# Optimization experiments

Hardware: AMD Instinct MI355X
Metric: run time of the kernel (lower is better)

The kernel has to match this reference:

```python
import jax, jax.numpy as jnp
import numpy as np

B = 524288
H = 64  # hidden_dim
D = 1   # input_dim


def setup_inputs() -> dict:
    key = jax.random.key(0)
    ks = jax.random.split(key, 16)
    s = 0.05
    inp = {
        "gradients": jax.random.normal(ks[0], (B, D), jnp.float32),
        "parameters": jax.random.normal(ks[1], (B, D), jnp.float32),
        "momentum": jax.random.normal(ks[2], (B, D), jnp.float32),
        "h0": jax.random.normal(ks[3], (B, H), jnp.float32),
        "c0": jax.random.normal(ks[4], (B, H), jnp.float32),
        # input_processor: Linear(3D->H), ReLU, Linear(H->H)
        "W1": jax.random.normal(ks[5], (H, 3 * D), jnp.float32) * s,
        "b1": jax.random.normal(ks[6], (H,), jnp.float32) * s,
        "W2": jax.random.normal(ks[7], (H, H), jnp.float32) * s,
        "b2": jax.random.normal(ks[8], (H,), jnp.float32) * s,
        # LSTM cell (PyTorch layout: gates stacked i,f,g,o -> 4H rows)
        "W_ih": jax.random.normal(ks[9], (4 * H, H), jnp.float32) * s,
        "W_hh": jax.random.normal(ks[10], (4 * H, H), jnp.float32) * s,
        "b_ih": jax.random.normal(ks[11], (4 * H,), jnp.float32) * s,
        "b_hh": jax.random.normal(ks[12], (4 * H,), jnp.float32) * s,
        # output_layer: Linear(H->D)
        "W_out": jax.random.normal(ks[13], (D, H), jnp.float32) * s,
        "b_out": jax.random.normal(ks[14], (D,), jnp.float32) * s,
    }
    return inp


def reference(gradients, parameters, momentum, h0, c0,
              W1, b1, W2, b2, W_ih, W_hh, b_ih, b_hh, W_out, b_out):
    # momentum update
    m = 0.9 * momentum + gradients                      # [B, D]
    feats = jnp.concatenate([gradients, parameters, m], axis=-1)  # [B, 3D]
    # small MLP
    x = jax.nn.relu(feats @ W1.T + b1) @ W2.T + b2      # [B, H]
    # single-step LSTM cell, PyTorch gate order i, f, g, o
    gates = x @ W_ih.T + b_ih + h0 @ W_hh.T + b_hh      # [B, 4H]
    i, f, g, o = jnp.split(gates, 4, axis=-1)
    c1 = jax.nn.sigmoid(f) * c0 + jax.nn.sigmoid(i) * jnp.tanh(g)
    h1 = jax.nn.sigmoid(o) * jnp.tanh(c1)               # [B, H]
    update = h1 @ W_out.T + b_out                       # [B, D]
    return update
```

## Files before the change

kernel.cpp:

```cpp
#include <hip/hip_runtime.h>
#include <hip/hip_bf16.h>
#include <stdint.h>


typedef __attribute__((ext_vector_type(8))) __bf16  bf16x8;
typedef __attribute__((ext_vector_type(4))) float   floatx4;

__device__ __forceinline__ unsigned short f2bf_bits(float x){
    unsigned u = __builtin_bit_cast(unsigned, x);
    u = u + 0x7fffu + ((u >> 16) & 1u);
    return (unsigned short)(u >> 16);
}
__device__ __forceinline__ unsigned pk2(float lo, float hi){
    return ((unsigned)f2bf_bits(hi) << 16) | (unsigned)f2bf_bits(lo);
}
__device__ __forceinline__ bf16x8 pack8(float4 a, float4 b){
    union { unsigned u[4]; bf16x8 v; } p;
    p.u[0] = pk2(a.x, a.y); p.u[1] = pk2(a.z, a.w);
    p.u[2] = pk2(b.x, b.y); p.u[3] = pk2(b.z, b.w);
    return p.v;
}
__device__ __forceinline__ float sigm(float x){
    float e = __builtin_amdgcn_exp2f(-1.442695041f * x);
    return __builtin_amdgcn_rcpf(1.0f + e);
}
__device__ __forceinline__ float tanh_fast(float x){
    float e = __builtin_amdgcn_exp2f(2.885390082f * x);
    return 1.0f - 2.0f * __builtin_amdgcn_rcpf(1.0f + e);
}

__global__ __launch_bounds__(256) void prep_kernel(
    const float* __restrict__ W2, const float* __restrict__ b2,
    const float* __restrict__ W_ih, const float* __restrict__ W_hh,
    const float* __restrict__ b_ih, const float* __restrict__ b_hh,
    unsigned short* __restrict__ wc, float* __restrict__ biasc)
{
    __shared__ float W2s[64*64];
    __shared__ float b2s[64];
    __shared__ float wihs[16*64];
    const int tid = threadIdx.x;
    const int b   = blockIdx.x;

    for (int i = 0; i < 4; i++){
        int idx = i*1024 + tid*4;
        *(float4*)(W2s + idx) = *(const float4*)(W2 + idx);
    }
    if (tid < 64) b2s[tid] = b2[tid];
    {
        int idx = tid*4;
        *(float4*)(wihs + idx) = *(const float4*)(W_ih + b*16*64 + idx);
    }
    __syncthreads();

    const int nl = tid >> 4;
    const int n  = b*16 + nl;
    const int jg = tid & 15;
    const int j  = jg*4;
    const int T  = n >> 4;

    float a0=0.f, a1=0.f, a2=0.f, a3=0.f;
    for (int h = 0; h < 64; h++){
        float wv = wihs[nl*64 + h];
        const float* w2r = W2s + h*64 + j;
        a0 += wv*w2r[0]; a1 += wv*w2r[1]; a2 += wv*w2r[2]; a3 += wv*w2r[3];
    }
    auto store4 = [&](int k, float v0, float v1, float v2, float v3){
        int s    = k >> 5;
        int lane = ((k >> 3) & 3)*16 + (n & 15);
        int off  = (T*4 + s)*512 + lane*8 + (k & 7);
        ushort4 v; v.x=f2bf_bits(v0); v.y=f2bf_bits(v1); v.z=f2bf_bits(v2); v.w=f2bf_bits(v3);
        *(ushort4*)(wc + off) = v;
    };
    store4(j, a0, a1, a2, a3);
    {
        const float* src = W_hh + n*64 + j;
        store4(64 + j, src[0], src[1], src[2], src[3]);
    }
    if (jg == 0){
        float s = b_ih[n] + b_hh[n];
        for (int h = 0; h < 64; h++) s += wihs[nl*64 + h]*b2s[h];
        biasc[n] = s;
    }
}

__global__ __launch_bounds__(512, 4) void main_kernel(
    const float* __restrict__ grad, const float* __restrict__ param,
    const float* __restrict__ mom,  const float* __restrict__ h0,
    const float* __restrict__ c0,   const float* __restrict__ W1,
    const float* __restrict__ b1,   const float* __restrict__ Wout,
    const float* __restrict__ bout,
    const unsigned short* __restrict__ wc, const float* __restrict__ biasc,
    float* __restrict__ out)
{
    __shared__ __align__(16) unsigned short wc_l[32768];
    __shared__ float  bias_l[256];
    __shared__ float4 w1p_l[64];

    const int tid  = threadIdx.x;
    const int lane = tid & 63;
    const int w    = tid >> 6;
    const int l15  = lane & 15;
    const int q    = lane >> 4;
    const long row0 = (long)blockIdx.x * 128;

    {
        const float4* src = (const float4*)wc;
        float4*       dst = (float4*)wc_l;
        #pragma unroll
        for (int i = 0; i < 8; i++)
            dst[i*512 + tid] = src[i*512 + tid];
    }
    if (tid < 256) bias_l[tid] = biasc[tid];
    if (tid >= 256 && tid < 320){
        int j = tid - 256;
        w1p_l[j] = make_float4(W1[j*3], W1[j*3+1], W1[j*3+2], b1[j]);
    }

    const long rA = row0 + w*16 + l15;
    float g = grad[rA], p = param[rA], mo = mom[rA];
    float m = 0.9f*mo + g;

    const float* hrow = h0 + rA*64;
    float4 ha = *(const float4*)(hrow + q*8);
    float4 hb = *(const float4*)(hrow + q*8 + 4);
    float4 hc = *(const float4*)(hrow + 32 + q*8);
    float4 hd = *(const float4*)(hrow + 32 + q*8 + 4);

    __syncthreads();

    float rv[16];
    #pragma unroll
    for (int s = 0; s < 2; s++)
        #pragma unroll
        for (int jj = 0; jj < 8; jj++){
            int j = s*32 + q*8 + jj;
            float4 wr = w1p_l[j];
            float v = fmaf(wr.x, g, fmaf(wr.y, p, fmaf(wr.z, m, wr.w)));
            rv[s*8+jj] = v > 0.f ? v : 0.f;
        }
    bf16x8 afr[4];
    afr[0] = pack8(make_float4(rv[0],rv[1],rv[2],rv[3]),
                   make_float4(rv[4],rv[5],rv[6],rv[7]));
    afr[1] = pack8(make_float4(rv[8],rv[9],rv[10],rv[11]),
                   make_float4(rv[12],rv[13],rv[14],rv[15]));
    afr[2] = pack8(ha, hb);
    afr[3] = pack8(hc, hd);

    floatx4 acc[16];
    #pragma unroll
    for (int T = 0; T < 16; T++){
        float bv = bias_l[T*16 + l15];
        const unsigned short* cb = wc_l + T*2048 + lane*8;
        bf16x8 b0 = *(const bf16x8*)(cb);
        bf16x8 b1f = *(const bf16x8*)(cb + 512);
        bf16x8 b2f = *(const bf16x8*)(cb + 1024);
        bf16x8 b3f = *(const bf16x8*)(cb + 1536);
        acc[T] = __builtin_amdgcn_mfma_f32_16x16x32_bf16(afr[0], b0,
                     (floatx4){bv, bv, bv, bv}, 0, 0, 0);
        acc[T] = __builtin_amdgcn_mfma_f32_16x16x32_bf16(afr[1], b1f, acc[T], 0, 0, 0);
        acc[T] = __builtin_amdgcn_mfma_f32_16x16x32_bf16(afr[2], b2f, acc[T], 0, 0, 0);
        acc[T] = __builtin_amdgcn_mfma_f32_16x16x32_bf16(afr[3], b3f, acc[T], 0, 0, 0);
    }

    const float* c0base = c0 + (row0 + w*16 + q*4)*64 + l15;
    float c0v[4][4];
    #pragma unroll
    for (int jh = 0; jh < 4; jh++)
        #pragma unroll
        for (int r = 0; r < 4; r++)
            c0v[jh][r] = c0base[r*64 + jh*16];

    float wo[4];
    #pragma unroll
    for (int jh = 0; jh < 4; jh++) wo[jh] = Wout[jh*16 + l15];
    const float bout0 = bout[0];

    float red[4] = {0.f, 0.f, 0.f, 0.f};
    #pragma unroll
    for (int jh = 0; jh < 4; jh++)
        #pragma unroll
        for (int r = 0; r < 4; r++){
            float iv = sigm(acc[jh][r]);
            float fv = sigm(acc[4+jh][r]);
            float gv = tanh_fast(acc[8+jh][r]);
            float ov = sigm(acc[12+jh][r]);
            float c1 = fmaf(fv, c0v[jh][r], iv*gv);
            float h1 = ov * tanh_fast(c1);
            red[r] = fmaf(h1, wo[jh], red[r]);
        }

    #pragma unroll
    for (int mset = 1; mset < 16; mset <<= 1)
        #pragma unroll
        for (int r = 0; r < 4; r++)
            red[r] += __shfl_xor(red[r], mset, 64);

    if (l15 == 0){
        long orow = row0 + w*16 + q*4;
        #pragma unroll
        for (int r = 0; r < 4; r++)
            out[orow + r] = red[r] + bout0;
    }
}

extern "C" void kernel_launch(void* const* d_in, const int* in_sizes, int n_in,
                              void* d_out, int out_size, void* d_ws, size_t ws_size,
                              hipStream_t stream)
{
    const float* grad  = (const float*)d_in[0];
    const float* param = (const float*)d_in[1];
    const float* mom   = (const float*)d_in[2];
    const float* h0    = (const float*)d_in[3];
    const float* c0    = (const float*)d_in[4];
    const float* W1    = (const float*)d_in[5];
    const float* b1    = (const float*)d_in[6];
    const float* W2    = (const float*)d_in[7];
    const float* b2    = (const float*)d_in[8];
    const float* W_ih  = (const float*)d_in[9];
    const float* W_hh  = (const float*)d_in[10];
    const float* b_ih  = (const float*)d_in[11];
    const float* b_hh  = (const float*)d_in[12];
    const float* Wout  = (const float*)d_in[13];
    const float* bout  = (const float*)d_in[14];

    unsigned short* wc = (unsigned short*)d_ws;
    float* biasc       = (float*)((char*)d_ws + 65536);

    prep_kernel<<<16, 256, 0, stream>>>(W2, b2, W_ih, W_hh, b_ih, b_hh, wc, biasc);

    const int nblocks = 524288 / 128;
    main_kernel<<<nblocks, 512, 0, stream>>>(grad, param, mom, h0, c0,
                                             W1, b1, Wout, bout, wc, biasc,
                                             (float*)d_out);
}
```

Baseline: 309.1 us.

## Make LSTM kernel persistent over row chunks with prefetch and per-hidden-slice gate MFMAs

The main kernel now uses 1024-thread blocks, each looping over four 256-row chunks. The next chunk's grad/param/mom/h0 loads are prefetched while the current chunk is computed. This amortizes the 64KB LDS weight staging over more rows and lets the gates be computed one hidden slice at a time (i,f,g,o per jh), so only four accumulators are live instead of sixteen, lowering register pressure. The bias is pre-scaled by the exp2 constant and folded into an fma, and bf16 packing uses a native vector convert. The risks are fewer blocks in the grid and a serialized jh loop that may expose MFMA and load latency.

```diff
diff --git a/kernel.cpp b/kernel.cpp
--- a/kernel.cpp
+++ b/kernel.cpp
@@ -4,6 +4,7 @@
 
 
 typedef __attribute__((ext_vector_type(8))) __bf16  bf16x8;
+typedef __attribute__((ext_vector_type(8))) float   f32x8;
 typedef __attribute__((ext_vector_type(4))) float   floatx4;
 
 __device__ __forceinline__ unsigned short f2bf_bits(float x){
@@ -11,22 +12,11 @@
     u = u + 0x7fffu + ((u >> 16) & 1u);
     return (unsigned short)(u >> 16);
 }
-__device__ __forceinline__ unsigned pk2(float lo, float hi){
-    return ((unsigned)f2bf_bits(hi) << 16) | (unsigned)f2bf_bits(lo);
-}
 __device__ __forceinline__ bf16x8 pack8(float4 a, float4 b){
-    union { unsigned u[4]; bf16x8 v; } p;
-    p.u[0] = pk2(a.x, a.y); p.u[1] = pk2(a.z, a.w);
-    p.u[2] = pk2(b.x, b.y); p.u[3] = pk2(b.z, b.w);
-    return p.v;
-}
-__device__ __forceinline__ float sigm(float x){
-    float e = __builtin_amdgcn_exp2f(-1.442695041f * x);
-    return __builtin_amdgcn_rcpf(1.0f + e);
-}
-__device__ __forceinline__ float tanh_fast(float x){
-    float e = __builtin_amdgcn_exp2f(2.885390082f * x);
-    return 1.0f - 2.0f * __builtin_amdgcn_rcpf(1.0f + e);
+    f32x8 t;
+    t[0]=a.x; t[1]=a.y; t[2]=a.z; t[3]=a.w;
+    t[4]=b.x; t[5]=b.y; t[6]=b.z; t[7]=b.w;
+    return __builtin_convertvector(t, bf16x8);
 }
 
 __global__ __launch_bounds__(256) void prep_kernel(
@@ -83,7 +73,7 @@
     }
 }
 
-__global__ __launch_bounds__(512, 4) void main_kernel(
+__global__ __launch_bounds__(1024, 4) void main_kernel(
     const float* __restrict__ grad, const float* __restrict__ param,
     const float* __restrict__ mom,  const float* __restrict__ h0,
     const float* __restrict__ c0,   const float* __restrict__ W1,
@@ -95,111 +85,157 @@
     __shared__ __align__(16) unsigned short wc_l[32768];
     __shared__ float  bias_l[256];
     __shared__ float4 w1p_l[64];
+    __shared__ float  wout_l[64];
 
     const int tid  = threadIdx.x;
     const int lane = tid & 63;
     const int w    = tid >> 6;
     const int l15  = lane & 15;
     const int q    = lane >> 4;
-    const long row0 = (long)blockIdx.x * 128;
 
     {
         const float4* src = (const float4*)wc;
         float4*       dst = (float4*)wc_l;
         #pragma unroll
-        for (int i = 0; i < 8; i++)
-            dst[i*512 + tid] = src[i*512 + tid];
-    }
-    if (tid < 256) bias_l[tid] = biasc[tid];
-    if (tid >= 256 && tid < 320){
+        for (int i = 0; i < 4; i++)
+            dst[i*1024 + tid] = src[i*1024 + tid];
+    }
+    if (tid < 256){
+        float sc = ((tid >> 6) == 2) ? 2.885390082f : -1.442695041f;
+        bias_l[tid] = sc * biasc[tid];
+    } else if (tid < 320){
         int j = tid - 256;
         w1p_l[j] = make_float4(W1[j*3], W1[j*3+1], W1[j*3+2], b1[j]);
-    }
-
-    const long rA = row0 + w*16 + l15;
-    float g = grad[rA], p = param[rA], mo = mom[rA];
-    float m = 0.9f*mo + g;
-
-    const float* hrow = h0 + rA*64;
-    float4 ha = *(const float4*)(hrow + q*8);
-    float4 hb = *(const float4*)(hrow + q*8 + 4);
-    float4 hc = *(const float4*)(hrow + 32 + q*8);
-    float4 hd = *(const float4*)(hrow + 32 + q*8 + 4);
+    } else if (tid < 384){
+        wout_l[tid - 320] = Wout[tid - 320];
+    }
+
+    const float bout0 = bout[0];
+    constexpr int NCH = 4;
+    const long blockBase = (long)blockIdx.x * (NCH * 256);
+
+    {
+        long rA = blockBase + w*16 + l15;
+    }
+    long rA0 = blockBase + w*16 + l15;
+    float g_r  = grad[rA0];
+    float p_r  = param[rA0];
+    float mo_r = mom[rA0];
+    const float* hr0 = h0 + rA0*64;
+    float4 ha = *(const float4*)(hr0 + q*8);
+    float4 hb = *(const float4*)(hr0 + q*8 + 4);
+    float4 hc = *(const float4*)(hr0 + 32 + q*8);
+    float4 hd = *(const float4*)(hr0 + 32 + q*8 + 4);
 
     __syncthreads();
 
-    float rv[16];
-    #pragma unroll
-    for (int s = 0; s < 2; s++)
+    const floatx4 zq = {0.f, 0.f, 0.f, 0.f};
+
+    #pragma unroll 1
+    for (int t = 0; t < NCH; ++t){
+        const long rowt = blockBase + t*256;
+
+        float m = fmaf(0.9f, mo_r, g_r);
+        f32x8 rlo, rhi;
         #pragma unroll
         for (int jj = 0; jj < 8; jj++){
-            int j = s*32 + q*8 + jj;
-            float4 wr = w1p_l[j];
-            float v = fmaf(wr.x, g, fmaf(wr.y, p, fmaf(wr.z, m, wr.w)));
-            rv[s*8+jj] = v > 0.f ? v : 0.f;
-        }
-    bf16x8 afr[4];
-    afr[0] = pack8(make_float4(rv[0],rv[1],rv[2],rv[3]),
-                   make_float4(rv[4],rv[5],rv[6],rv[7]));
-    afr[1] = pack8(make_float4(rv[8],rv[9],rv[10],rv[11]),
-                   make_float4(rv[12],rv[13],rv[14],rv[15]));
-    afr[2] = pack8(ha, hb);
-    afr[3] = pack8(hc, hd);
-
-    floatx4 acc[16];
-    #pragma unroll
-    for (int T = 0; T < 16; T++){
-        float bv = bias_l[T*16 + l15];
-        const unsigned short* cb = wc_l + T*2048 + lane*8;
-        bf16x8 b0 = *(const bf16x8*)(cb);
-        bf16x8 b1f = *(const bf16x8*)(cb + 512);
-        bf16x8 b2f = *(const bf16x8*)(cb + 1024);
-        bf16x8 b3f = *(const bf16x8*)(cb + 1536);
-        acc[T] = __builtin_amdgcn_mfma_f32_16x16x32_bf16(afr[0], b0,
-                     (floatx4){bv, bv, bv, bv}, 0, 0, 0);
-        acc[T] = __builtin_amdgcn_mfma_f32_16x16x32_bf16(afr[1], b1f, acc[T], 0, 0, 0);
-        acc[T] = __builtin_amdgcn_mfma_f32_16x16x32_bf16(afr[2], b2f, acc[T], 0, 0, 0);
-        acc[T] = __builtin_amdgcn_mfma_f32_16x16x32_bf16(afr[3], b3f, acc[T], 0, 0, 0);
-    }
-
-    const float* c0base = c0 + (row0 + w*16 + q*4)*64 + l15;
-    float c0v[4][4];
-    #pragma unroll
-    for (int jh = 0; jh < 4; jh++)
-        #pragma unroll
-        for (int r = 0; r < 4; r++)
-            c0v[jh][r] = c0base[r*64 + jh*16];
-
-    float wo[4];
-    #pragma unroll
-    for (int jh = 0; jh < 4; jh++) wo[jh] = Wout[jh*16 + l15];
-    const float bout0 = bout[0];
-
-    float red[4] = {0.f, 0.f, 0.f, 0.f};
-    #pragma unroll
-    for (int jh = 0; jh < 4; jh++)
-        #pragma unroll
-        for (int r = 0; r < 4; r++){
-            float iv = sigm(acc[jh][r]);
-            float fv = sigm(acc[4+jh][r]);
-            float gv = tanh_fast(acc[8+jh][r]);
-            float ov = sigm(acc[12+jh][r]);
-            float c1 = fmaf(fv, c0v[jh][r], iv*gv);
-            float h1 = ov * tanh_fast(c1);
-            red[r] = fmaf(h1, wo[jh], red[r]);
-        }
-
-    #pragma unroll
-    for (int mset = 1; mset < 16; mset <<= 1)
-        #pragma unroll
-        for (int r = 0; r < 4; r++)
-            red[r] += __shfl_xor(red[r], mset, 64);
-
-    if (l15 == 0){
-        long orow = row0 + w*16 + q*4;
-        #pragma unroll
-        for (int r = 0; r < 4; r++)
-            out[orow + r] = red[r] + bout0;
+            float4 wr = w1p_l[q*8 + jj];
+            float v = fmaf(wr.x, g_r, fmaf(wr.y, p_r, fmaf(wr.z, m, wr.w)));
+            rlo[jj] = v > 0.f ? v : 0.f;
+        }
+        #pragma unroll
+        for (int jj = 0; jj < 8; jj++){
+            float4 wr = w1p_l[32 + q*8 + jj];
+            float v = fmaf(wr.x, g_r, fmaf(wr.y, p_r, fmaf(wr.z, m, wr.w)));
+            rhi[jj] = v > 0.f ? v : 0.f;
+        }
+        bf16x8 afr0 = __builtin_convertvector(rlo, bf16x8);
+        bf16x8 afr1 = __builtin_convertvector(rhi, bf16x8);
+        bf16x8 afr2 = pack8(ha, hb);
+        bf16x8 afr3 = pack8(hc, hd);
+
+        if (t != NCH-1){
+            long rAn = rowt + 256 + w*16 + l15;
+            g_r  = grad[rAn];
+            p_r  = param[rAn];
+            mo_r = mom[rAn];
+            const float* hrn = h0 + rAn*64;
+            ha = *(const float4*)(hrn + q*8);
+            hb = *(const float4*)(hrn + q*8 + 4);
+            hc = *(const float4*)(hrn + 32 + q*8);
+            hd = *(const float4*)(hrn + 32 + q*8 + 4);
+        }
+
+        const float* c0b = c0 + (rowt + w*16 + q*4)*64 + l15;
+        float red[4] = {0.f, 0.f, 0.f, 0.f};
+
+        #pragma unroll 1
+        for (int jh = 0; jh < 4; ++jh){
+            const int jh16 = jh << 4;
+
+            float c0v[4];
+            c0v[0] = c0b[jh16];
+            c0v[1] = c0b[jh16 + 64];
+            c0v[2] = c0b[jh16 + 128];
+            c0v[3] = c0b[jh16 + 192];
+
+            float bsi = bias_l[jh16 + l15];
+            float bsf = bias_l[jh16 + l15 + 64];
+            float bsg = bias_l[jh16 + l15 + 128];
+            float bso = bias_l[jh16 + l15 + 192];
+            float wo  = wout_l[jh16 + l15];
+
+            const unsigned short* cb = wc_l + jh*2048 + lane*8;
+            #define BFRAG(o) (*(const bf16x8*)(cb + (o)))
+            floatx4 xi, xf, xg, xo;
+            xi = __builtin_amdgcn_mfma_f32_16x16x32_bf16(afr0, BFRAG(0),         zq, 0,0,0);
+            xi = __builtin_amdgcn_mfma_f32_16x16x32_bf16(afr1, BFRAG(512),       xi, 0,0,0);
+            xi = __builtin_amdgcn_mfma_f32_16x16x32_bf16(afr2, BFRAG(1024),      xi, 0,0,0);
+            xi = __builtin_amdgcn_mfma_f32_16x16x32_bf16(afr3, BFRAG(1536),      xi, 0,0,0);
+            xf = __builtin_amdgcn_mfma_f32_16x16x32_bf16(afr0, BFRAG(8192),      zq, 0,0,0);
+            xf = __builtin_amdgcn_mfma_f32_16x16x32_bf16(afr1, BFRAG(8192+512),  xf, 0,0,0);
+            xf = __builtin_amdgcn_mfma_f32_16x16x32_bf16(afr2, BFRAG(8192+1024), xf, 0,0,0);
+            xf = __builtin_amdgcn_mfma_f32_16x16x32_bf16(afr3, BFRAG(8192+1536), xf, 0,0,0);
+            xg = __builtin_amdgcn_mfma_f32_16x16x32_bf16(afr0, BFRAG(16384),     zq, 0,0,0);
+            xg = __builtin_amdgcn_mfma_f32_16x16x32_bf16(afr1, BFRAG(16384+512), xg, 0,0,0);
+            xg = __builtin_amdgcn_mfma_f32_16x16x32_bf16(afr2, BFRAG(16384+1024),xg, 0,0,0);
+            xg = __builtin_amdgcn_mfma_f32_16x16x32_bf16(afr3, BFRAG(16384+1536),xg, 0,0,0);
+            xo = __builtin_amdgcn_mfma_f32_16x16x32_bf16(afr0, BFRAG(24576),     zq, 0,0,0);
+            xo = __builtin_amdgcn_mfma_f32_16x16x32_bf16(afr1, BFRAG(24576+512), xo, 0,0,0);
+            xo = __builtin_amdgcn_mfma_f32_16x16x32_bf16(afr2, BFRAG(24576+1024),xo, 0,0,0);
+            xo = __builtin_amdgcn_mfma_f32_16x16x32_bf16(afr3, BFRAG(24576+1536),xo, 0,0,0);
+            #undef BFRAG
+
+            #pragma unroll
+            for (int r = 0; r < 4; ++r){
+                float ei = __builtin_amdgcn_exp2f(fmaf(-1.442695041f, xi[r], bsi));
+                float iv = __builtin_amdgcn_rcpf(1.0f + ei);
+                float ef = __builtin_amdgcn_exp2f(fmaf(-1.442695041f, xf[r], bsf));
+                float fv = __builtin_amdgcn_rcpf(1.0f + ef);
+                float eo = __builtin_amdgcn_exp2f(fmaf(-1.442695041f, xo[r], bso));
+                float ov = __builtin_amdgcn_rcpf(1.0f + eo);
+                float eg = __builtin_amdgcn_exp2f(fmaf( 2.885390082f, xg[r], bsg));
+                float gv = fmaf(-2.0f, __builtin_amdgcn_rcpf(1.0f + eg), 1.0f);
+                float c1 = fmaf(fv, c0v[r], iv*gv);
+                float ec = __builtin_amdgcn_exp2f(2.885390082f * c1);
+                float tv = fmaf(-2.0f, __builtin_amdgcn_rcpf(1.0f + ec), 1.0f);
+                float h1 = ov * tv;
+                red[r] = fmaf(h1, wo, red[r]);
+            }
+        }
+
+        #pragma unroll
+        for (int mset = 1; mset < 16; mset <<= 1)
+            #pragma unroll
+            for (int r = 0; r < 4; r++)
+                red[r] += __shfl_xor(red[r], mset, 64);
+
+        if (l15 == 0){
+            long orow = rowt + w*16 + q*4;
+            #pragma unroll
+            for (int r = 0; r < 4; r++)
+                out[orow + r] = red[r] + bout0;
+        }
     }
 }
 
@@ -228,8 +264,8 @@
 
     prep_kernel<<<16, 256, 0, stream>>>(W2, b2, W_ih, W_hh, b_ih, b_hh, wc, biasc);
 
-    const int nblocks = 524288 / 128;
-    main_kernel<<<nblocks, 512, 0, stream>>>(grad, param, mom, h0, c0,
-                                             W1, b1, Wout, bout, wc, biasc,
-                                             (float*)d_out);
-}
+    const int nblocks = 524288 / (4 * 256);
+    main_kernel<<<nblocks, 1024, 0, stream>>>(grad, param, mom, h0, c0,
+                                              W1, b1, Wout, bout, wc, biasc,
+                                              (float*)d_out);
+}
```

New measurement: 339.6 us. 9.8% more time.

## Interleave per-hidden-chunk MFMA gates with LSTM epilogue and prefetch c0

Applied to the files above, without the earlier changes.

Restructures the main kernel so the 16 gate accumulators are no longer all computed before the epilogue. Instead it runs four phases, each computing the i/f/g/o tiles for one 16-column hidden chunk and then immediately applying the activations, with c0 loads for later chunks prefetched early. The gate bias is pre-scaled by the exp2 constant in shared memory and folded into an fma, Wout moves to LDS, and bf16 packing uses the native vector convert. This cuts live accumulator registers and may let memory and MFMA overlap with transcendental work, at the cost of more serialized dependency chains per phase.

```diff
diff --git a/kernel.cpp b/kernel.cpp
--- a/kernel.cpp
+++ b/kernel.cpp
@@ -4,6 +4,7 @@
 
 
 typedef __attribute__((ext_vector_type(8))) __bf16  bf16x8;
+typedef __attribute__((ext_vector_type(8))) float   f32x8;
 typedef __attribute__((ext_vector_type(4))) float   floatx4;
 
 __device__ __forceinline__ unsigned short f2bf_bits(float x){
@@ -11,22 +12,11 @@
     u = u + 0x7fffu + ((u >> 16) & 1u);
     return (unsigned short)(u >> 16);
 }
-__device__ __forceinline__ unsigned pk2(float lo, float hi){
-    return ((unsigned)f2bf_bits(hi) << 16) | (unsigned)f2bf_bits(lo);
-}
 __device__ __forceinline__ bf16x8 pack8(float4 a, float4 b){
-    union { unsigned u[4]; bf16x8 v; } p;
-    p.u[0] = pk2(a.x, a.y); p.u[1] = pk2(a.z, a.w);
-    p.u[2] = pk2(b.x, b.y); p.u[3] = pk2(b.z, b.w);
-    return p.v;
-}
-__device__ __forceinline__ float sigm(float x){
-    float e = __builtin_amdgcn_exp2f(-1.442695041f * x);
-    return __builtin_amdgcn_rcpf(1.0f + e);
-}
-__device__ __forceinline__ float tanh_fast(float x){
-    float e = __builtin_amdgcn_exp2f(2.885390082f * x);
-    return 1.0f - 2.0f * __builtin_amdgcn_rcpf(1.0f + e);
+    f32x8 t;
+    t[0]=a.x; t[1]=a.y; t[2]=a.z; t[3]=a.w;
+    t[4]=b.x; t[5]=b.y; t[6]=b.z; t[7]=b.w;
+    return __builtin_convertvector(t, bf16x8);
 }
 
 __global__ __launch_bounds__(256) void prep_kernel(
@@ -95,6 +85,7 @@
     __shared__ __align__(16) unsigned short wc_l[32768];
     __shared__ float  bias_l[256];
     __shared__ float4 w1p_l[64];
+    __shared__ float  wout_l[64];
 
     const int tid  = threadIdx.x;
     const int lane = tid & 63;
@@ -110,84 +101,114 @@
         for (int i = 0; i < 8; i++)
             dst[i*512 + tid] = src[i*512 + tid];
     }
-    if (tid < 256) bias_l[tid] = biasc[tid];
-    if (tid >= 256 && tid < 320){
+    if (tid < 256){
+        float sc = ((tid >> 6) == 2) ? 2.885390082f : -1.442695041f;
+        bias_l[tid] = sc * biasc[tid];
+    } else if (tid < 320){
         int j = tid - 256;
         w1p_l[j] = make_float4(W1[j*3], W1[j*3+1], W1[j*3+2], b1[j]);
+    } else if (tid < 384){
+        wout_l[tid - 320] = Wout[tid - 320];
     }
 
     const long rA = row0 + w*16 + l15;
     float g = grad[rA], p = param[rA], mo = mom[rA];
-    float m = 0.9f*mo + g;
-
     const float* hrow = h0 + rA*64;
     float4 ha = *(const float4*)(hrow + q*8);
     float4 hb = *(const float4*)(hrow + q*8 + 4);
     float4 hc = *(const float4*)(hrow + 32 + q*8);
     float4 hd = *(const float4*)(hrow + 32 + q*8 + 4);
+    const float bout0 = bout[0];
 
     __syncthreads();
 
-    float rv[16];
-    #pragma unroll
-    for (int s = 0; s < 2; s++)
-        #pragma unroll
-        for (int jj = 0; jj < 8; jj++){
-            int j = s*32 + q*8 + jj;
-            float4 wr = w1p_l[j];
-            float v = fmaf(wr.x, g, fmaf(wr.y, p, fmaf(wr.z, m, wr.w)));
-            rv[s*8+jj] = v > 0.f ? v : 0.f;
-        }
-    bf16x8 afr[4];
-    afr[0] = pack8(make_float4(rv[0],rv[1],rv[2],rv[3]),
-                   make_float4(rv[4],rv[5],rv[6],rv[7]));
-    afr[1] = pack8(make_float4(rv[8],rv[9],rv[10],rv[11]),
-                   make_float4(rv[12],rv[13],rv[14],rv[15]));
-    afr[2] = pack8(ha, hb);
-    afr[3] = pack8(hc, hd);
-
-    floatx4 acc[16];
-    #pragma unroll
-    for (int T = 0; T < 16; T++){
-        float bv = bias_l[T*16 + l15];
-        const unsigned short* cb = wc_l + T*2048 + lane*8;
-        bf16x8 b0 = *(const bf16x8*)(cb);
-        bf16x8 b1f = *(const bf16x8*)(cb + 512);
-        bf16x8 b2f = *(const bf16x8*)(cb + 1024);
-        bf16x8 b3f = *(const bf16x8*)(cb + 1536);
-        acc[T] = __builtin_amdgcn_mfma_f32_16x16x32_bf16(afr[0], b0,
-                     (floatx4){bv, bv, bv, bv}, 0, 0, 0);
-        acc[T] = __builtin_amdgcn_mfma_f32_16x16x32_bf16(afr[1], b1f, acc[T], 0, 0, 0);
-        acc[T] = __builtin_amdgcn_mfma_f32_16x16x32_bf16(afr[2], b2f, acc[T], 0, 0, 0);
-        acc[T] = __builtin_amdgcn_mfma_f32_16x16x32_bf16(afr[3], b3f, acc[T], 0, 0, 0);
-    }
-
-    const float* c0base = c0 + (row0 + w*16 + q*4)*64 + l15;
-    float c0v[4][4];
-    #pragma unroll
-    for (int jh = 0; jh < 4; jh++)
-        #pragma unroll
-        for (int r = 0; r < 4; r++)
-            c0v[jh][r] = c0base[r*64 + jh*16];
-
-    float wo[4];
-    #pragma unroll
-    for (int jh = 0; jh < 4; jh++) wo[jh] = Wout[jh*16 + l15];
-    const float bout0 = bout[0];
+    float m = fmaf(0.9f, mo, g);
+    f32x8 rlo, rhi;
+    #pragma unroll
+    for (int jj = 0; jj < 8; jj++){
+        float4 wr = w1p_l[q*8 + jj];
+        float v = fmaf(wr.x, g, fmaf(wr.y, p, fmaf(wr.z, m, wr.w)));
+        rlo[jj] = v > 0.f ? v : 0.f;
+    }
+    #pragma unroll
+    for (int jj = 0; jj < 8; jj++){
+        float4 wr = w1p_l[32 + q*8 + jj];
+        float v = fmaf(wr.x, g, fmaf(wr.y, p, fmaf(wr.z, m, wr.w)));
+        rhi[jj] = v > 0.f ? v : 0.f;
+    }
+    bf16x8 afr0 = __builtin_convertvector(rlo, bf16x8);
+    bf16x8 afr1 = __builtin_convertvector(rhi, bf16x8);
+    bf16x8 afr2 = pack8(ha, hb);
+    bf16x8 afr3 = pack8(hc, hd);
+
+    const float* c0b = c0 + (rA & ~15L)*64 + (q*4)*64 + l15;
+    float c0v0[4], c0v1[4], c0v2[4], c0v3[4];
+    #pragma unroll
+    for (int r = 0; r < 4; ++r) c0v0[r] = c0b[r*64];
+    #pragma unroll
+    for (int r = 0; r < 4; ++r) c0v1[r] = c0b[r*64 + 16];
 
     float red[4] = {0.f, 0.f, 0.f, 0.f};
-    #pragma unroll
-    for (int jh = 0; jh < 4; jh++)
-        #pragma unroll
-        for (int r = 0; r < 4; r++){
-            float iv = sigm(acc[jh][r]);
-            float fv = sigm(acc[4+jh][r]);
-            float gv = tanh_fast(acc[8+jh][r]);
-            float ov = sigm(acc[12+jh][r]);
-            float c1 = fmaf(fv, c0v[jh][r], iv*gv);
-            float h1 = ov * tanh_fast(c1);
-            red[r] = fmaf(h1, wo[jh], red[r]);
-        }
+    const floatx4 zq = {0.f, 0.f, 0.f, 0.f};
+
+#define GATE1(cb, Gofs, d)                                                    \
+{                                                                             \
+    bf16x8 t0 = *(const bf16x8*)((cb) + (Gofs));                              \
+    bf16x8 t1 = *(const bf16x8*)((cb) + (Gofs) + 512);                        \
+    bf16x8 t2 = *(const bf16x8*)((cb) + (Gofs) + 1024);                       \
+    bf16x8 t3 = *(const bf16x8*)((cb) + (Gofs) + 1536);                       \
+    d = __builtin_amdgcn_mfma_f32_16x16x32_bf16(afr0, t0, zq, 0,0,0);         \
+    d = __builtin_amdgcn_mfma_f32_16x16x32_bf16(afr1, t1, d,  0,0,0);         \
+    d = __builtin_amdgcn_mfma_f32_16x16x32_bf16(afr2, t2, d,  0,0,0);         \
+    d = __builtin_amdgcn_mfma_f32_16x16x32_bf16(afr3, t3, d,  0,0,0);         \
+}
+
+#define EPILOG(XI, XF, XG, XO, CV, BI, BF, BG, BO, WO)                        \
+    _Pragma("unroll")                                                         \
+    for (int r = 0; r < 4; ++r){                                              \
+        float ei = __builtin_amdgcn_exp2f(fmaf(-1.442695041f, XI[r], BI));    \
+        float iv = __builtin_amdgcn_rcpf(1.0f + ei);                          \
+        float ef = __builtin_amdgcn_exp2f(fmaf(-1.442695041f, XF[r], BF));    \
+        float fv = __builtin_amdgcn_rcpf(1.0f + ef);                          \
+        float eo = __builtin_amdgcn_exp2f(fmaf(-1.442695041f, XO[r], BO));    \
+        float ov = __builtin_amdgcn_rcpf(1.0f + eo);                          \
+        float eg = __builtin_amdgcn_exp2f(fmaf( 2.885390082f, XG[r], BG));    \
+        float gv = fmaf(-2.0f, __builtin_amdgcn_rcpf(1.0f + eg), 1.0f);       \
+        float c1 = fmaf(fv, CV[r], iv*gv);                                    \
+        float ec = __builtin_amdgcn_exp2f(2.885390082f * c1);                 \
+        float tv = fmaf(-2.0f, __builtin_amdgcn_rcpf(1.0f + ec), 1.0f);       \
+        red[r] = fmaf(ov * tv, WO, red[r]);                                   \
+    }
+
+#define PHASE(JH, CV, PRE_CV, DO_PRE)                                         \
+{                                                                             \
+    if (DO_PRE){                                                              \
+        _Pragma("unroll")                                                     \
+        for (int r = 0; r < 4; ++r) PRE_CV[r] = c0b[r*64 + ((JH)+2)*16];      \
+    }                                                                         \
+    const int jh16 = (JH) << 4;                                               \
+    const float bsi = bias_l[jh16 + l15];                                     \
+    const float bsf = bias_l[jh16 + l15 + 64];                                \
+    const float bsg = bias_l[jh16 + l15 + 128];                               \
+    const float bso = bias_l[jh16 + l15 + 192];                               \
+    const float wo  = wout_l[jh16 + l15];                                     \
+    const unsigned short* cbp = wc_l + (JH)*2048 + lane*8;                    \
+    floatx4 xi, xf, xg, xo;                                                   \
+    GATE1(cbp, 0,     xi)                                                     \
+    GATE1(cbp, 8192,  xf)                                                     \
+    GATE1(cbp, 16384, xg)                                                     \
+    GATE1(cbp, 24576, xo)                                                     \
+    EPILOG(xi, xf, xg, xo, CV, bsi, bsf, bsg, bso, wo)                        \
+}
+
+    PHASE(0, c0v0, c0v2, 1)
+    PHASE(1, c0v1, c0v3, 1)
+    PHASE(2, c0v2, c0v0, 0)
+    PHASE(3, c0v3, c0v0, 0)
+
+#undef PHASE
+#undef EPILOG
+#undef GATE1
 
     #pragma unroll
     for (int mset = 1; mset < 16; mset <<= 1)
```

Measured after the change: 311.0 us. About the same (+0.6%).
